# Optimization experiments

Hardware: AMD Instinct MI355X
Metric: run time of the kernel (lower is better)

The kernel has to match this reference:

```python
import jax, jax.numpy as jnp
import numpy as np

DIM = 192
HEADS = 8
B = 8
HH = 128
WW = 128
EPS_BN = 1e-5
EPS_NORM = 1e-12


def _bn(x, g, b, m, v):
    # inference-mode BatchNorm2d over channel axis 1, x: (B,C,H,W)
    inv = g / jnp.sqrt(v + EPS_BN)
    return x * inv[None, :, None, None] + (b - m * inv)[None, :, None, None]


def _gelu(x):
    return jax.nn.gelu(x, approximate=False)


def setup_inputs() -> dict:
    key = jax.random.key(0)
    ks = jax.random.split(key, 16)
    d, h8, h16 = DIM, DIM // 8, DIM // 16
    N = HH * WW
    s = 0.02
    inp = {
        "x": jax.random.normal(ks[0], (B, N, d), jnp.float32),
        "H": HH,
        "W": WW,
        "w_qkv": jax.random.normal(ks[1], (d, 3 * d), jnp.float32) * s,
        "temperature": jnp.ones((HEADS, 1, 1), jnp.float32),
        "dw_w": jax.random.normal(ks[2], (d, 1, 3, 3), jnp.float32) * s,
        "dw_b": jnp.zeros((d,), jnp.float32),
        "bn1_g": jnp.ones((d,), jnp.float32), "bn1_b": jnp.zeros((d,), jnp.float32),
        "bn1_m": jnp.zeros((d,), jnp.float32), "bn1_v": jnp.ones((d,), jnp.float32),
        "ci_w1": jax.random.normal(ks[3], (h8, d), jnp.float32) * s,
        "ci_b1": jnp.zeros((h8,), jnp.float32),
        "bn2_g": jnp.ones((h8,), jnp.float32), "bn2_b": jnp.zeros((h8,), jnp.float32),
        "bn2_m": jnp.zeros((h8,), jnp.float32), "bn2_v": jnp.ones((h8,), jnp.float32),
        "ci_w2": jax.random.normal(ks[4], (d, h8), jnp.float32) * s,
        "ci_b2": jnp.zeros((d,), jnp.float32),
        "si_w1": jax.random.normal(ks[5], (h16, d), jnp.float32) * s,
        "si_b1": jnp.zeros((h16,), jnp.float32),
        "bn3_g": jnp.ones((h16,), jnp.float32), "bn3_b": jnp.zeros((h16,), jnp.float32),
        "bn3_m": jnp.zeros((h16,), jnp.float32), "bn3_v": jnp.ones((h16,), jnp.float32),
        "si_w2": jax.random.normal(ks[6], (1, h16), jnp.float32) * s,
        "si_b2": jnp.zeros((1,), jnp.float32),
        "proj_w": jax.random.normal(ks[7], (d, d), jnp.float32) * s,
        "proj_b": jnp.zeros((d,), jnp.float32),
    }
    return inp


def reference(x, H, W, w_qkv, temperature, dw_w, dw_b,
              bn1_g, bn1_b, bn1_m, bn1_v,
              ci_w1, ci_b1, bn2_g, bn2_b, bn2_m, bn2_v, ci_w2, ci_b2,
              si_w1, si_b1, bn3_g, bn3_b, bn3_m, bn3_v, si_w2, si_b2,
              proj_w, proj_b):
    Bn, N, C = x.shape
    hd = C // HEADS
    # qkv projection (no bias), split into heads: (3,B,h,N,hd)
    qkv = (x @ w_qkv).reshape(Bn, N, 3, HEADS, hd).transpose(2, 0, 3, 1, 4)
    q = qkv[0].transpose(0, 1, 3, 2)  # (B,h,hd,N)
    k = qkv[1].transpose(0, 1, 3, 2)
    v = qkv[2].transpose(0, 1, 3, 2)
    v_img = v.reshape(Bn, C, N).reshape(Bn, C, H, W)
    # L2-normalize along token axis (F.normalize eps=1e-12)
    q = q / jnp.clip(jnp.linalg.norm(q, axis=-1, keepdims=True), EPS_NORM)
    k = k / jnp.clip(jnp.linalg.norm(k, axis=-1, keepdims=True), EPS_NORM)
    attn = jnp.einsum('bhcn,bhdn->bhcd', q, k) * temperature  # (B,h,hd,hd)
    attn = jax.nn.softmax(attn, axis=-1)
    att_x = jnp.einsum('bhcd,bhdn->bhcn', attn, v)  # (B,h,hd,N)
    att_x = att_x.transpose(0, 3, 1, 2).reshape(Bn, N, C)
    # depthwise conv branch: 3x3 dw conv + BN + GELU
    conv_x = jax.lax.conv_general_dilated(
        v_img, dw_w, window_strides=(1, 1), padding='SAME',
        dimension_numbers=('NCHW', 'OIHW', 'NCHW'), feature_group_count=C)
    conv_x = _gelu(_bn(conv_x + dw_b[None, :, None, None], bn1_g, bn1_b, bn1_m, bn1_v))
    # channel interaction: SE gate computed from attention branch
    att_img = att_x.transpose(0, 2, 1).reshape(Bn, C, H, W)
    pooled = jnp.mean(att_img, axis=(2, 3), keepdims=True)  # (B,C,1,1)
    cm = jnp.einsum('bcij,oc->boij', pooled, ci_w1) + ci_b1[None, :, None, None]
    cm = _gelu(_bn(cm, bn2_g, bn2_b, bn2_m, bn2_v))
    channel_map = jnp.einsum('bcij,oc->boij', cm, ci_w2) + ci_b2[None, :, None, None]
    # spatial interaction: gate computed from conv branch
    sm = jnp.einsum('bchw,oc->bohw', conv_x, si_w1) + si_b1[None, :, None, None]
    sm = _gelu(_bn(sm, bn3_g, bn3_b, bn3_m, bn3_v))
    spatial_map = jnp.einsum('bchw,oc->bohw', sm, si_w2) + si_b2[None, :, None, None]
    spatial_map = spatial_map.transpose(0, 2, 3, 1).reshape(Bn, N, 1)
    # cross gating
    att_x = att_x * jax.nn.sigmoid(spatial_map)
    conv_x = conv_x * jax.nn.sigmoid(channel_map)
    conv_x = conv_x.transpose(0, 2, 3, 1).reshape(Bn, N, C)
    out = (att_x + conv_x) @ proj_w + proj_b
    return out
```

## Files before the change

### kernel.cpp

```cpp
#include <hip/hip_runtime.h>
#include <math.h>

#define Bb 8
#define Cc 192
#define NHEADS 8
#define HDim 24
#define Him 128
#define Wim 128
#define Ntok 16384
#define EPSBN 1e-5f

typedef __bf16 bf16x8 __attribute__((ext_vector_type(8)));
typedef float  f32x4  __attribute__((ext_vector_type(4)));

static __device__ __forceinline__ float gelu_f(float v) {
    return 0.5f * v * (1.0f + erff(v * 0.70710678118654752f));
}
static __device__ __forceinline__ float sigmoid_f(float v) {
    return 1.0f / (1.0f + expf(-v));
}
static __device__ __forceinline__ void split8(const float* xv, bf16x8& h8, bf16x8& l8) {
#pragma unroll
    for (int j = 0; j < 8; ++j) {
        float v = xv[j];
        __bf16 h = (__bf16)v;
        h8[j] = h;
        l8[j] = (__bf16)(v - (float)h);
    }
}

__global__ __launch_bounds__(256) void k_wprep(const float* __restrict__ w,
                                               __bf16* __restrict__ wt)
{
    int idx = blockIdx.x * 256 + threadIdx.x;
    if (idx >= 36864) return;
    int k = idx / 192, c = idx % 192;
    float v = w[k * 576 + 384 + c];
    __bf16 h = (__bf16)v;
    __bf16 l = (__bf16)(v - (float)h);
    wt[c * 192 + k] = h;
    wt[36864 + c * 192 + k] = l;
}

__global__ __launch_bounds__(256, 2) void k_xtx(const float* __restrict__ x,
                                                float* __restrict__ xpart)
{
    const int t = threadIdx.x;
    const int lane = t & 63, wave = t >> 6;
    const int chunk = blockIdx.x;
    const int b = blockIdx.y;
    const int n0 = chunk * 256;
    const int m16 = lane & 15, q = lane >> 4;
    const int rq = (wave & 1) * 6;
    const int cq = (wave >> 1) * 6;

    f32x4 acc[6][6];
#pragma unroll
    for (int i = 0; i < 6; ++i)
#pragma unroll
        for (int j = 0; j < 6; ++j)
#pragma unroll
            for (int r = 0; r < 4; ++r) acc[i][j][r] = 0.f;

    const float* xb = x + ((size_t)b * Ntok + n0) * 192;

    for (int kt = 0; kt < 8; ++kt) {
        const float* base = xb + (size_t)(kt * 32 + q * 8) * 192 + m16;
#pragma unroll
        for (int rb = 0; rb < 2; ++rb) {
            bf16x8 fah[3], fal[3];
#pragma unroll
            for (int g = 0; g < 3; ++g) {
                const float* src = base + (rq + rb * 3 + g) * 16;
                float xv[8];
#pragma unroll
                for (int j = 0; j < 8; ++j) xv[j] = src[(size_t)j * 192];
                split8(xv, fah[g], fal[g]);
            }
#pragma unroll
            for (int cb = 0; cb < 2; ++cb) {
                bf16x8 fbh[3], fbl[3];
#pragma unroll
                for (int g = 0; g < 3; ++g) {
                    const float* src = base + (cq + cb * 3 + g) * 16;
                    float xv[8];
#pragma unroll
                    for (int j = 0; j < 8; ++j) xv[j] = src[(size_t)j * 192];
                    split8(xv, fbh[g], fbl[g]);
                }
#pragma unroll
                for (int ti = 0; ti < 3; ++ti)
#pragma unroll
                    for (int tj = 0; tj < 3; ++tj) {
                        f32x4& a = acc[rb * 3 + ti][cb * 3 + tj];
                        a = __builtin_amdgcn_mfma_f32_16x16x32_bf16(fah[ti], fbh[tj], a, 0, 0, 0);
                        a = __builtin_amdgcn_mfma_f32_16x16x32_bf16(fah[ti], fbl[tj], a, 0, 0, 0);
                        a = __builtin_amdgcn_mfma_f32_16x16x32_bf16(fal[ti], fbh[tj], a, 0, 0, 0);
                    }
            }
        }
    }
    float* op = xpart + ((size_t)b * 64 + chunk) * 36864;
#pragma unroll
    for (int ti = 0; ti < 6; ++ti)
#pragma unroll
        for (int tj = 0; tj < 6; ++tj) {
            const int row0 = (rq + ti) * 16 + q * 4;
            const int col = (cq + tj) * 16 + m16;
#pragma unroll
            for (int j = 0; j < 4; ++j)
                op[(size_t)(row0 + j) * 192 + col] = acc[ti][tj][j];
        }
}

__global__ __launch_bounds__(256) void k_xred(const float* __restrict__ xpart,
                                              float* __restrict__ XtX)
{
    const int b = blockIdx.y;
    const int e = blockIdx.x * 256 + threadIdx.x;
    const float* p = xpart + (size_t)b * 64 * 36864 + e;
    float s = 0.f;
#pragma unroll
    for (int c = 0; c < 64; ++c) s += p[(size_t)c * 36864];
    XtX[(size_t)b * 36864 + e] = s;
}

__global__ __launch_bounds__(256) void k_gram2(const float* __restrict__ XtX,
                                               const float* __restrict__ w_qkv,
                                               float* __restrict__ gram,
                                               float* __restrict__ ssq_q,
                                               float* __restrict__ ssq_k)
{
    __shared__ float wq[192][24];
    __shared__ float wk[192][24];
    __shared__ float U[192][24];
    __shared__ float V[192][24];
    const int b = blockIdx.x, h = blockIdx.y, t = threadIdx.x;
    for (int e = t; e < 4608; e += 256) {
        int k = e / 24, c = e % 24;
        wq[k][c] = w_qkv[k * 576 + h * 24 + c];
        wk[k][c] = w_qkv[k * 576 + 192 + h * 24 + c];
    }
    __syncthreads();
    if (t < 192) {
        const float* xr = XtX + (size_t)b * 36864 + (size_t)t * 192;
        float u[24], v[24];
#pragma unroll
        for (int c = 0; c < 24; ++c) { u[c] = 0.f; v[c] = 0.f; }
        for (int k4 = 0; k4 < 48; ++k4) {
            float4 x4 = *(const float4*)(xr + k4 * 4);
#pragma unroll
            for (int kk = 0; kk < 4; ++kk) {
                float xv = (&x4.x)[kk];
                int k = k4 * 4 + kk;
#pragma unroll
                for (int c = 0; c < 24; ++c) {
                    u[c] = fmaf(xv, wq[k][c], u[c]);
                    v[c] = fmaf(xv, wk[k][c], v[c]);
                }
            }
        }
#pragma unroll
        for (int c = 0; c < 24; ++c) { U[t][c] = u[c]; V[t][c] = v[c]; }
    }
    __syncthreads();
    for (int o = t; o < 576; o += 256) {
        int c = o / 24, d = o % 24;
        float g = 0.f;
        for (int r = 0; r < 192; ++r) g = fmaf(wq[r][c], V[r][d], g);
        gram[(size_t)(b * NHEADS + h) * 576 + o] = g;
    }
    if (t < 24) {
        float s = 0.f;
        for (int r = 0; r < 192; ++r) s = fmaf(wq[r][t], U[r][t], s);
        ssq_q[b * Cc + h * HDim + t] = s;
    } else if (t < 48) {
        int c = t - 24;
        float s = 0.f;
        for (int r = 0; r < 192; ++r) s = fmaf(wk[r][c], V[r][c], s);
        ssq_k[b * Cc + h * HDim + c] = s;
    }
}

__global__ __launch_bounds__(256, 2) void k_qkv_mfma(const float* __restrict__ x,
                                                     const __bf16* __restrict__ wt,
                                                     float* __restrict__ vout,
                                                     float* __restrict__ vsum)
{
    __shared__ __align__(16) __bf16 Ah[128 * 40];
    __shared__ __align__(16) __bf16 Al[128 * 40];
    __shared__ __align__(16) __bf16 Bh[192 * 40];
    __shared__ __align__(16) __bf16 Bl[192 * 40];

    const int t = threadIdx.x;
    const int lane = t & 63, wave = t >> 6;
    const int n0 = blockIdx.x * 128;
    const int b = blockIdx.y;
    const int row_base = (wave & 1) * 64;
    const int col_base = (wave >> 1) * 96;
    const int m16 = lane & 15, q = lane >> 4;

    f32x4 acc[4][6];
#pragma unroll
    for (int rt = 0; rt < 4; ++rt)
#pragma unroll
        for (int ct = 0; ct < 6; ++ct)
#pragma unroll
            for (int j = 0; j < 4; ++j) acc[rt][ct][j] = 0.f;

    const int ar = t >> 1, ahalf = t & 1;
    const float* xrow = x + ((size_t)b * Ntok + n0 + ar) * Cc + ahalf * 16;

    for (int kc = 0; kc < 6; ++kc) {
        {
            const float4* xp4 = (const float4*)(xrow + kc * 32);
            float xv[16];
            float4 u;
            u = xp4[0]; xv[0] = u.x; xv[1] = u.y; xv[2]  = u.z; xv[3]  = u.w;
            u = xp4[1]; xv[4] = u.x; xv[5] = u.y; xv[6]  = u.z; xv[7]  = u.w;
            u = xp4[2]; xv[8] = u.x; xv[9] = u.y; xv[10] = u.z; xv[11] = u.w;
            u = xp4[3]; xv[12] = u.x; xv[13] = u.y; xv[14] = u.z; xv[15] = u.w;
            bf16x8 vh0, vh1, vl0, vl1;
            split8(xv, vh0, vl0);
            split8(xv + 8, vh1, vl1);
            const int o = ar * 40 + ahalf * 16;
            *(bf16x8*)&Ah[o] = vh0; *(bf16x8*)&Ah[o + 8] = vh1;
            *(bf16x8*)&Al[o] = vl0; *(bf16x8*)&Al[o + 8] = vl1;
        }
#pragma unroll
        for (int i = 0; i < 3; ++i) {
            int f = i * 256 + t;
            int n = f >> 2, k8 = (f & 3) << 3;
            const __bf16* src = wt + (size_t)n * 192 + kc * 32 + k8;
            bf16x8 vh = *(const bf16x8*)src;
            bf16x8 vl = *(const bf16x8*)(src + 36864);
            *(bf16x8*)&Bh[n * 40 + k8] = vh;
            *(bf16x8*)&Bl[n * 40 + k8] = vl;
        }
        __syncthreads();

        bf16x8 fah[4], fal[4], fbh[6], fbl[6];
#pragma unroll
        for (int rt = 0; rt < 4; ++rt) {
            int o = (row_base + rt * 16 + m16) * 40 + q * 8;
            fah[rt] = *(const bf16x8*)&Ah[o];
            fal[rt] = *(const bf16x8*)&Al[o];
        }
#pragma unroll
        for (int ct = 0; ct < 6; ++ct) {
            int o = (col_base + ct * 16 + m16) * 40 + q * 8;
            fbh[ct] = *(const bf16x8*)&Bh[o];
            fbl[ct] = *(const bf16x8*)&Bl[o];
        }
#pragma unroll
        for (int rt = 0; rt < 4; ++rt)
#pragma unroll
            for (int ct = 0; ct < 6; ++ct) {
                acc[rt][ct] = __builtin_amdgcn_mfma_f32_16x16x32_bf16(
                    fah[rt], fbh[ct], acc[rt][ct], 0, 0, 0);
                acc[rt][ct] = __builtin_amdgcn_mfma_f32_16x16x32_bf16(
                    fah[rt], fbl[ct], acc[rt][ct], 0, 0, 0);
                acc[rt][ct] = __builtin_amdgcn_mfma_f32_16x16x32_bf16(
                    fal[rt], fbh[ct], acc[rt][ct], 0, 0, 0);
            }
        __syncthreads();
    }

    const size_t obase = (size_t)b * Cc * (size_t)Ntok;
#pragma unroll
    for (int rt = 0; rt < 4; ++rt)
#pragma unroll
        for (int ct = 0; ct < 6; ++ct) {
            int token = n0 + row_base + rt * 16 + q * 4;
            int col = col_base + ct * 16 + m16;
            float4 o = make_float4(acc[rt][ct][0], acc[rt][ct][1],
                                   acc[rt][ct][2], acc[rt][ct][3]);
            *(float4*)(vout + obase + (size_t)col * Ntok + token) = o;
        }

#pragma unroll
    for (int ct = 0; ct < 6; ++ct) {
        float s = 0.f;
#pragma unroll
        for (int rt = 0; rt < 4; ++rt)
            s += acc[rt][ct][0] + acc[rt][ct][1] + acc[rt][ct][2] + acc[rt][ct][3];
        s += __shfl_xor(s, 16, 64);
        s += __shfl_xor(s, 32, 64);
        if (q == 0)
            atomicAdd(vsum + b * Cc + col_base + ct * 16 + m16, s);
    }
}

__global__ __launch_bounds__(256) void k_attn(const float* __restrict__ gram,
                                              const float* __restrict__ ssq_q,
                                              const float* __restrict__ ssq_k,
                                              const float* __restrict__ temperature,
                                              const float* __restrict__ vmean,
                                              const float* __restrict__ ci_w1,
                                              const float* __restrict__ ci_b1,
                                              const float* __restrict__ bn2_g,
                                              const float* __restrict__ bn2_b,
                                              const float* __restrict__ bn2_m,
                                              const float* __restrict__ bn2_v,
                                              const float* __restrict__ ci_w2,
                                              const float* __restrict__ ci_b2,
                                              float* __restrict__ attn,
                                              float* __restrict__ sig_ch)
{
    __shared__ float pooled[192];
    __shared__ float cmv[24];
    const int b = blockIdx.x, t = threadIdx.x;
    if (t < 192) {
        int h = t / 24, c = t % 24;
        const float* gp = gram + (size_t)(b * NHEADS + h) * 576 + c * 24;
        float qn = fmaxf(sqrtf(ssq_q[b * Cc + h * HDim + c]), 1e-12f);
        float temp = temperature[h];
        float logit[24];
        float m = -1e30f;
#pragma unroll
        for (int d = 0; d < 24; ++d) {
            float kn = fmaxf(sqrtf(ssq_k[b * Cc + h * HDim + d]), 1e-12f);
            float l = gp[d] / (qn * kn) * temp;
            logit[d] = l; m = fmaxf(m, l);
        }
        float s = 0.f;
#pragma unroll
        for (int d = 0; d < 24; ++d) { float e = expf(logit[d] - m); logit[d] = e; s += e; }
        float inv = 1.f / s;
        float pool = 0.f;
        float* ap = attn + (size_t)(b * NHEADS + h) * 576 + c * 24;
#pragma unroll
        for (int d = 0; d < 24; ++d) {
            float a = logit[d] * inv;
            ap[d] = a;
            pool = fmaf(a, vmean[b * Cc + h * HDim + d], pool);
        }
        pooled[h * 24 + c] = pool * (1.0f / (float)Ntok);
    }
    __syncthreads();
    if (t < 24) {
        float z = ci_b1[t];
        for (int c = 0; c < 192; ++c) z = fmaf(ci_w1[t * 192 + c], pooled[c], z);
        float sc = bn2_g[t] / sqrtf(bn2_v[t] + EPSBN);
        z = z * sc + (bn2_b[t] - bn2_m[t] * sc);
        cmv[t] = gelu_f(z);
    }
    __syncthreads();
    if (t < 192) {
        float z = ci_b2[t];
#pragma unroll
        for (int o = 0; o < 24; ++o) z = fmaf(ci_w2[t * 24 + o], cmv[o], z);
        sig_ch[b * Cc + t] = sigmoid_f(z);
    }
}

__global__ __launch_bounds__(192) void k_pprep(const float* __restrict__ attn,
                                               const float* __restrict__ sig_ch,
                                               const float* __restrict__ proj_w,
                                               __bf16* __restrict__ Pt)
{
    const int b = blockIdx.x, part = blockIdx.y, j = threadIdx.x;
    __bf16* base = Pt + (size_t)b * (2 * 73728);
    if (part < 8) {
        const int h = part;
        __shared__ float at[576];
        for (int e = j; e < 576; e += 192) at[e] = attn[(size_t)(b * 8 + h) * 576 + e];
        __syncthreads();
        float pr[24];
#pragma unroll
        for (int cl = 0; cl < 24; ++cl) pr[cl] = proj_w[(h * 24 + cl) * 192 + j];
        float s[24];
#pragma unroll
        for (int d = 0; d < 24; ++d) s[d] = 0.f;
#pragma unroll
        for (int cl = 0; cl < 24; ++cl) {
            float a = pr[cl];
#pragma unroll
            for (int d = 0; d < 24; ++d) s[d] = fmaf(a, at[cl * 24 + d], s[d]);
        }
#pragma unroll
        for (int d = 0; d < 24; ++d) {
            float v = s[d];
            __bf16 hi = (__bf16)v;
            base[j * 384 + h * 24 + d] = hi;
            base[73728 + j * 384 + h * 24 + d] = (__bf16)(v - (float)hi);
        }
    } else {
        __shared__ float sch_s[192];
        sch_s[j] = sig_ch[b * Cc + j];
        __syncthreads();
        for (int ch = 0; ch < 192; ++ch) {
            float v = sch_s[ch] * proj_w[ch * 192 + j];
            __bf16 hi = (__bf16)v;
            base[j * 384 + 192 + ch] = hi;
            base[73728 + j * 384 + 192 + ch] = (__bf16)(v - (float)hi);
        }
    }
}

__global__ __launch_bounds__(256) void k_conv(const float* __restrict__ vbuf,
                                              const float* __restrict__ dw_w,
                                              const float* __restrict__ dw_b,
                                              const float* __restrict__ bn1_g,
                                              const float* __restrict__ bn1_b,
                                              const float* __restrict__ bn1_m,
                                              const float* __restrict__ bn1_v,
                                              float* __restrict__ convx)
{
    __shared__ float vh[8][10][130];
    __shared__ float dww[8 * 9];
    __shared__ float scl[8], shf[8];
    const int t = threadIdx.x;
    const int y0 = blockIdx.x * 8;
    const int ch0 = blockIdx.y * 8;
    const int b = blockIdx.z;

    if (t < 72) {
        dww[t] = dw_w[ch0 * 9 + t];
    } else if (t < 80) {
        int c = t - 72, ch = ch0 + c;
        float sc = bn1_g[ch] / sqrtf(bn1_v[ch] + EPSBN);
        scl[c] = sc;
        shf[c] = (dw_b[ch] - bn1_m[ch]) * sc + bn1_b[ch];
    } else if (t < 160) {
        int e = t - 80;
        int ch = e / 10, r = e % 10;
        vh[ch][r][0] = 0.f;
        vh[ch][r][129] = 0.f;
    }
    for (int e = t; e < 8 * 10 * 128; e += 256) {
        int ch = e / 1280, rem = e - ch * 1280;
        int r = rem >> 7, xc = rem & 127;
        int gy = y0 - 1 + r;
        float v = 0.f;
        if (gy >= 0 && gy < Him)
            v = vbuf[((size_t)b * Cc + ch0 + ch) * Ntok + gy * Wim + xc];
        vh[ch][r][xc + 1] = v;
    }
    __syncthreads();

    const int xc = t & 127, half = t >> 7;
#pragma unroll
    for (int ch = 0; ch < 8; ++ch) {
        const float w0 = dww[ch * 9 + 0], w1 = dww[ch * 9 + 1], w2 = dww[ch * 9 + 2];
        const float w3 = dww[ch * 9 + 3], w4 = dww[ch * 9 + 4], w5 = dww[ch * 9 + 5];
        const float w6 = dww[ch * 9 + 6], w7 = dww[ch * 9 + 7], w8 = dww[ch * 9 + 8];
        const float sc = scl[ch], sh = shf[ch];
        float* op = convx + ((size_t)b * Cc + ch0 + ch) * Ntok + (size_t)y0 * Wim + xc;
#pragma unroll
        for (int rr = 0; rr < 4; ++rr) {
            int r = half * 4 + rr;
            const float* r0 = &vh[ch][r][xc];
            const float* r1 = &vh[ch][r + 1][xc];
            const float* r2 = &vh[ch][r + 2][xc];
            float conv = r0[0] * w0 + r0[1] * w1 + r0[2] * w2
                       + r1[0] * w3 + r1[1] * w4 + r1[2] * w5
                       + r2[0] * w6 + r2[1] * w7 + r2[2] * w8;
            op[(size_t)r * Wim] = gelu_f(conv * sc + sh);
        }
    }
}

__global__ __launch_bounds__(256, 2) void k_final_mfma(const float* __restrict__ vbuf,
                                                       const float* __restrict__ convx,
                                                       const __bf16* __restrict__ Pt,
                                                       const float* __restrict__ si_w1,
                                                       const float* __restrict__ si_b1,
                                                       const float* __restrict__ bn3_g,
                                                       const float* __restrict__ bn3_b,
                                                       const float* __restrict__ bn3_m,
                                                       const float* __restrict__ bn3_v,
                                                       const float* __restrict__ si_w2,
                                                       const float* __restrict__ si_b2,
                                                       const float* __restrict__ proj_b,
                                                       float* __restrict__ out)
{
    __shared__ __align__(16) __bf16 Ah[128 * 40];
    __shared__ __align__(16) __bf16 Al[128 * 40];
    __shared__ __align__(16) __bf16 Bh[192 * 40];
    __shared__ __align__(16) __bf16 Bl[192 * 40];
    __shared__ float smbuf[128][17];
    __shared__ float ssp_s[128];

    const int t = threadIdx.x;
    const int lane = t & 63, wave = t >> 6;
    const int n0 = blockIdx.x * 128;
    const int b = blockIdx.y;
    const int row_base = (wave & 1) * 64;
    const int col_base = (wave >> 1) * 96;
    const int m16 = lane & 15, q = lane >> 4;

    const int an = t & 127;
    const int akh = (t >> 7) & 1;
    const __bf16* ptb = Pt + (size_t)b * (2 * 73728);

    f32x4 acc[4][6];
#pragma unroll
    for (int rt = 0; rt < 4; ++rt)
#pragma unroll
        for (int ct = 0; ct < 6; ++ct)
#pragma unroll
            for (int j = 0; j < 4; ++j) acc[rt][ct][j] = 0.f;
    f32x4 accS[4];
#pragma unroll
    for (int rt = 0; rt < 4; ++rt)
#pragma unroll
        for (int j = 0; j < 4; ++j) accS[rt][j] = 0.f;

    for (int phase = 0; phase < 2; ++phase) {
        if (phase == 1) {
#pragma unroll
            for (int rt = 0; rt < 4; ++rt) {
                int row = row_base + rt * 16 + q * 4;
#pragma unroll
                for (int j = 0; j < 4; ++j)
                    smbuf[row + j][m16] = accS[rt][j];
            }
            __syncthreads();
            if (t < 128) {
                float sp = si_b2[0];
#pragma unroll
                for (int o = 0; o < 12; ++o) {
                    float z = smbuf[t][o] + si_b1[o];
                    float sc = bn3_g[o] / sqrtf(bn3_v[o] + EPSBN);
                    z = z * sc + (bn3_b[o] - bn3_m[o] * sc);
                    sp = fmaf(si_w2[o], gelu_f(z), sp);
                }
                ssp_s[t] = sigmoid_f(sp);
            }
            __syncthreads();
        }
        for (int ki = 0; ki < 6; ++ki) {
            const int kc = (phase == 0) ? (ki + 6) : ki;
            {
                const int ch0 = ki * 32 + akh * 16;
                const float* src;
                float scale;
                if (phase == 0) {
                    src = convx + ((size_t)b * Cc + ch0) * Ntok + n0 + an;
                    scale = 1.f;
                } else {
                    src = vbuf + ((size_t)b * Cc + ch0) * Ntok + n0 + an;
                    scale = ssp_s[an];
                }
                float xv[16];
#pragma unroll
                for (int jj = 0; jj < 16; ++jj)
                    xv[jj] = src[(size_t)jj * Ntok] * scale;
                bf16x8 vh0, vl0, vh1, vl1;
                split8(xv, vh0, vl0);
                split8(xv + 8, vh1, vl1);
                const int o = an * 40 + akh * 16;
                *(bf16x8*)&Ah[o] = vh0; *(bf16x8*)&Ah[o + 8] = vh1;
                *(bf16x8*)&Al[o] = vl0; *(bf16x8*)&Al[o + 8] = vl1;
            }
#pragma unroll
            for (int i = 0; i < 3; ++i) {
                int f = i * 256 + t;
                int col = f >> 2, k8 = (f & 3) << 3;
                const __bf16* sp = ptb + (size_t)col * 384 + kc * 32 + k8;
                bf16x8 vh = *(const bf16x8*)sp;
                bf16x8 vl = *(const bf16x8*)(sp + 73728);
                *(bf16x8*)&Bh[col * 40 + k8] = vh;
                *(bf16x8*)&Bl[col * 40 + k8] = vl;
            }
            __syncthreads();

            bf16x8 fah[4], fal[4], fbh[6], fbl[6];
#pragma unroll
            for (int rt = 0; rt < 4; ++rt) {
                int o = (row_base + rt * 16 + m16) * 40 + q * 8;
                fah[rt] = *(const bf16x8*)&Ah[o];
                fal[rt] = *(const bf16x8*)&Al[o];
            }
#pragma unroll
            for (int ct = 0; ct < 6; ++ct) {
                int o = (col_base + ct * 16 + m16) * 40 + q * 8;
                fbh[ct] = *(const bf16x8*)&Bh[o];
            }
#pragma unroll
            for (int rt = 0; rt < 4; ++rt)
#pragma unroll
                for (int ct = 0; ct < 6; ++ct) {
                    acc[rt][ct] = __builtin_amdgcn_mfma_f32_16x16x32_bf16(
                        fah[rt], fbh[ct], acc[rt][ct], 0, 0, 0);
                    acc[rt][ct] = __builtin_amdgcn_mfma_f32_16x16x32_bf16(
                        fal[rt], fbh[ct], acc[rt][ct], 0, 0, 0);
                }
#pragma unroll
            for (int ct = 0; ct < 6; ++ct) {
                int o = (col_base + ct * 16 + m16) * 40 + q * 8;
                fbl[ct] = *(const bf16x8*)&Bl[o];
            }
#pragma unroll
            for (int rt = 0; rt < 4; ++rt)
#pragma unroll
                for (int ct = 0; ct < 6; ++ct)
                    acc[rt][ct] = __builtin_amdgcn_mfma_f32_16x16x32_bf16(
                        fah[rt], fbl[ct], acc[rt][ct], 0, 0, 0);

            if (phase == 0) {
                bf16x8 w1h, w1l;
                if (m16 < 12) {
                    const float* wp = si_w1 + m16 * 192 + ki * 32 + q * 8;
                    float wv[8];
                    float4 u0 = *(const float4*)wp, u1 = *(const float4*)(wp + 4);
                    wv[0] = u0.x; wv[1] = u0.y; wv[2] = u0.z; wv[3] = u0.w;
                    wv[4] = u1.x; wv[5] = u1.y; wv[6] = u1.z; wv[7] = u1.w;
                    split8(wv, w1h, w1l);
                } else {
#pragma unroll
                    for (int j = 0; j < 8; ++j) { w1h[j] = (__bf16)0.f; w1l[j] = (__bf16)0.f; }
                }
#pragma unroll
                for (int rt = 0; rt < 4; ++rt) {
                    accS[rt] = __builtin_amdgcn_mfma_f32_16x16x32_bf16(
                        fah[rt], w1h, accS[rt], 0, 0, 0);
                    accS[rt] = __builtin_amdgcn_mfma_f32_16x16x32_bf16(
                        fal[rt], w1h, accS[rt], 0, 0, 0);
                    accS[rt] = __builtin_amdgcn_mfma_f32_16x16x32_bf16(
                        fah[rt], w1l, accS[rt], 0, 0, 0);
                }
            }
            __syncthreads();
        }
    }

    float* ob = out + ((size_t)b * Ntok + n0) * Cc;
#pragma unroll
    for (int ct = 0; ct < 6; ++ct) {
        const int col = col_base + ct * 16 + m16;
        const float pbv = proj_b[col];
#pragma unroll
        for (int rt = 0; rt < 4; ++rt) {
            const int row = row_base + rt * 16 + q * 4;
#pragma unroll
            for (int j = 0; j < 4; ++j)
                ob[(size_t)(row + j) * Cc + col] = acc[rt][ct][j] + pbv;
        }
    }
}

extern "C" void kernel_launch(void* const* d_in, const int* in_sizes, int n_in,
                              void* d_out, int out_size, void* d_ws, size_t ws_size,
                              hipStream_t stream)
{
    const float* x      = (const float*)d_in[0];
    const float* w_qkv  = (const float*)d_in[3];
    const float* temperature = (const float*)d_in[4];
    const float* dw_w   = (const float*)d_in[5];
    const float* dw_b   = (const float*)d_in[6];
    const float* bn1_g  = (const float*)d_in[7];
    const float* bn1_b  = (const float*)d_in[8];
    const float* bn1_m  = (const float*)d_in[9];
    const float* bn1_v  = (const float*)d_in[10];
    const float* ci_w1  = (const float*)d_in[11];
    const float* ci_b1  = (const float*)d_in[12];
    const float* bn2_g  = (const float*)d_in[13];
    const float* bn2_b  = (const float*)d_in[14];
    const float* bn2_m  = (const float*)d_in[15];
    const float* bn2_v  = (const float*)d_in[16];
    const float* ci_w2  = (const float*)d_in[17];
    const float* ci_b2  = (const float*)d_in[18];
    const float* si_w1  = (const float*)d_in[19];
    const float* si_b1  = (const float*)d_in[20];
    const float* bn3_g  = (const float*)d_in[21];
    const float* bn3_b  = (const float*)d_in[22];
    const float* bn3_m  = (const float*)d_in[23];
    const float* bn3_v  = (const float*)d_in[24];
    const float* si_w2  = (const float*)d_in[25];
    const float* si_b2  = (const float*)d_in[26];
    const float* proj_w = (const float*)d_in[27];
    const float* proj_b = (const float*)d_in[28];

    float* ws = (float*)d_ws;
    const size_t BCN = (size_t)Bb * Cc * Ntok;
    float* vbuf  = ws;
    float* convx = ws + BCN;
    __bf16* Pt   = (__bf16*)(ws + 2 * BCN);
    float* xpart = ws + 2 * BCN + 589824;
    float* XtX   = xpart + 18874368;
    float* gram  = XtX + 294912;
    float* ssq_q = gram + 36864;
    float* ssq_k = ssq_q + 1536;
    float* vmean = ssq_k + 1536;
    float* attn  = vmean + 1536;
    float* sig_ch = attn + 36864;
    float* out = (float*)d_out;

    __bf16* wt = (__bf16*)(out + BCN - 36864);

    hipMemsetAsync(vmean, 0, 1536 * sizeof(float), stream);

    k_wprep<<<dim3(144), 256, 0, stream>>>(w_qkv, wt);
    k_xtx<<<dim3(64, Bb), 256, 0, stream>>>(x, xpart);
    k_xred<<<dim3(144, Bb), 256, 0, stream>>>(xpart, XtX);
    k_gram2<<<dim3(Bb, NHEADS), 256, 0, stream>>>(XtX, w_qkv, gram, ssq_q, ssq_k);
    k_qkv_mfma<<<dim3(Ntok / 128, Bb), 256, 0, stream>>>(x, wt, vbuf, vmean);
    k_attn<<<dim3(Bb), 256, 0, stream>>>(gram, ssq_q, ssq_k, temperature, vmean,
                                         ci_w1, ci_b1, bn2_g, bn2_b, bn2_m, bn2_v,
                                         ci_w2, ci_b2, attn, sig_ch);
    k_pprep<<<dim3(Bb, 9), 192, 0, stream>>>(attn, sig_ch, proj_w, Pt);
    k_conv<<<dim3(Him / 8, Cc / 8, Bb), 256, 0, stream>>>(
        vbuf, dw_w, dw_b, bn1_g, bn1_b, bn1_m, bn1_v, convx);
    k_final_mfma<<<dim3(Ntok / 128, Bb), 256, 0, stream>>>(
        vbuf, convx, Pt, si_w1, si_b1, bn3_g, bn3_b, bn3_m, bn3_v,
        si_w2, si_b2, proj_b, out);
}
```

Baseline: 610.3 us.

## Stage XtX tiles through LDS with coalesced loads; vectorize depthwise conv

The X^T X kernel now loads x with coalesced float4 reads, splits each value into bf16 hi/lo once, and stores the result transposed in shared memory. The MFMA fragments are then read from shared memory instead of as strided scalar global loads that were each split several times. Each block covers 512 tokens instead of 256, which halves the partial-sum buffer and the reduction work but launches fewer blocks. The depthwise conv drops its shared-memory halo tile: each thread reads its three rows directly with float4 loads and writes four outputs as one float4.

```diff
diff --git a/kernel.cpp b/kernel.cpp
--- a/kernel.cpp
+++ b/kernel.cpp
@@ -11,6 +11,7 @@
 #define EPSBN 1e-5f
 
 typedef __bf16 bf16x8 __attribute__((ext_vector_type(8)));
+typedef __bf16 bf16x2 __attribute__((ext_vector_type(2)));
 typedef float  f32x4  __attribute__((ext_vector_type(4)));
 
 static __device__ __forceinline__ float gelu_f(float v) {
@@ -45,11 +46,13 @@
 __global__ __launch_bounds__(256, 2) void k_xtx(const float* __restrict__ x,
                                                 float* __restrict__ xpart)
 {
+    __shared__ __align__(16) __bf16 Th[192 * 40];
+    __shared__ __align__(16) __bf16 Tl[192 * 40];
     const int t = threadIdx.x;
     const int lane = t & 63, wave = t >> 6;
     const int chunk = blockIdx.x;
     const int b = blockIdx.y;
-    const int n0 = chunk * 256;
+    const int n0 = chunk * 512;
     const int m16 = lane & 15, q = lane >> 4;
     const int rq = (wave & 1) * 6;
     const int cq = (wave >> 1) * 6;
@@ -62,31 +65,61 @@
 #pragma unroll
             for (int r = 0; r < 4; ++r) acc[i][j][r] = 0.f;
 
+    int u0 = t, u1 = t + 256, u2 = t + 512;
+    const int ch4_0 = (u0 % 48) * 4, tk_0 = (u0 / 48) * 2;
+    const int ch4_1 = (u1 % 48) * 4, tk_1 = (u1 / 48) * 2;
+    const int ch4_2 = (u2 % 48) * 4, tk_2 = (u2 / 48) * 2;
     const float* xb = x + ((size_t)b * Ntok + n0) * 192;
-
-    for (int kt = 0; kt < 8; ++kt) {
-        const float* base = xb + (size_t)(kt * 32 + q * 8) * 192 + m16;
+    const float* p0 = xb + (size_t)tk_0 * 192 + ch4_0;
+    const float* p1 = xb + (size_t)tk_1 * 192 + ch4_1;
+    const float* p2 = xb + (size_t)tk_2 * 192 + ch4_2;
+    const int o0 = ch4_0 * 40 + tk_0;
+    const int o1 = ch4_1 * 40 + tk_1;
+    const int o2 = ch4_2 * 40 + tk_2;
+
+    for (int ks = 0; ks < 16; ++ks) {
+        __syncthreads();
+        {
+            const float* pp[3] = { p0, p1, p2 };
+            const int oo[3] = { o0, o1, o2 };
+#pragma unroll
+            for (int j = 0; j < 3; ++j) {
+                const float* p = pp[j] + (size_t)ks * 32 * 192;
+                float4 a = *(const float4*)p;
+                float4 c = *(const float4*)(p + 192);
+#pragma unroll
+                for (int cix = 0; cix < 4; ++cix) {
+                    float v0 = (&a.x)[cix], v1 = (&c.x)[cix];
+                    __bf16 h0 = (__bf16)v0, h1 = (__bf16)v1;
+                    __bf16 l0 = (__bf16)(v0 - (float)h0);
+                    __bf16 l1 = (__bf16)(v1 - (float)h1);
+                    int o = oo[j] + cix * 40;
+                    bf16x2 hp; hp[0] = h0; hp[1] = h1;
+                    bf16x2 lp; lp[0] = l0; lp[1] = l1;
+                    *(bf16x2*)&Th[o] = hp;
+                    *(bf16x2*)&Tl[o] = lp;
+                }
+            }
+        }
+        __syncthreads();
+
 #pragma unroll
         for (int rb = 0; rb < 2; ++rb) {
             bf16x8 fah[3], fal[3];
 #pragma unroll
             for (int g = 0; g < 3; ++g) {
-                const float* src = base + (rq + rb * 3 + g) * 16;
-                float xv[8];
-#pragma unroll
-                for (int j = 0; j < 8; ++j) xv[j] = src[(size_t)j * 192];
-                split8(xv, fah[g], fal[g]);
+                int o = ((rq + rb * 3 + g) * 16 + m16) * 40 + q * 8;
+                fah[g] = *(const bf16x8*)&Th[o];
+                fal[g] = *(const bf16x8*)&Tl[o];
             }
 #pragma unroll
             for (int cb = 0; cb < 2; ++cb) {
                 bf16x8 fbh[3], fbl[3];
 #pragma unroll
                 for (int g = 0; g < 3; ++g) {
-                    const float* src = base + (cq + cb * 3 + g) * 16;
-                    float xv[8];
-#pragma unroll
-                    for (int j = 0; j < 8; ++j) xv[j] = src[(size_t)j * 192];
-                    split8(xv, fbh[g], fbl[g]);
+                    int o = ((cq + cb * 3 + g) * 16 + m16) * 40 + q * 8;
+                    fbh[g] = *(const bf16x8*)&Th[o];
+                    fbl[g] = *(const bf16x8*)&Tl[o];
                 }
 #pragma unroll
                 for (int ti = 0; ti < 3; ++ti)
@@ -100,7 +133,7 @@
             }
         }
     }
-    float* op = xpart + ((size_t)b * 64 + chunk) * 36864;
+    float* op = xpart + ((size_t)b * 32 + chunk) * 36864;
 #pragma unroll
     for (int ti = 0; ti < 6; ++ti)
 #pragma unroll
@@ -118,10 +151,10 @@
 {
     const int b = blockIdx.y;
     const int e = blockIdx.x * 256 + threadIdx.x;
-    const float* p = xpart + (size_t)b * 64 * 36864 + e;
+    const float* p = xpart + (size_t)b * 32 * 36864 + e;
     float s = 0.f;
 #pragma unroll
-    for (int c = 0; c < 64; ++c) s += p[(size_t)c * 36864];
+    for (int c = 0; c < 32; ++c) s += p[(size_t)c * 36864];
     XtX[(size_t)b * 36864 + e] = s;
 }
 
@@ -407,8 +440,7 @@
                                               const float* __restrict__ bn1_v,
                                               float* __restrict__ convx)
 {
-    __shared__ float vh[8][10][130];
-    __shared__ float dww[8 * 9];
+    __shared__ float dww[72];
     __shared__ float scl[8], shf[8];
     const int t = threadIdx.x;
     const int y0 = blockIdx.x * 8;
@@ -422,42 +454,45 @@
         float sc = bn1_g[ch] / sqrtf(bn1_v[ch] + EPSBN);
         scl[c] = sc;
         shf[c] = (dw_b[ch] - bn1_m[ch]) * sc + bn1_b[ch];
-    } else if (t < 160) {
-        int e = t - 80;
-        int ch = e / 10, r = e % 10;
-        vh[ch][r][0] = 0.f;
-        vh[ch][r][129] = 0.f;
-    }
-    for (int e = t; e < 8 * 10 * 128; e += 256) {
-        int ch = e / 1280, rem = e - ch * 1280;
-        int r = rem >> 7, xc = rem & 127;
-        int gy = y0 - 1 + r;
-        float v = 0.f;
-        if (gy >= 0 && gy < Him)
-            v = vbuf[((size_t)b * Cc + ch0 + ch) * Ntok + gy * Wim + xc];
-        vh[ch][r][xc + 1] = v;
     }
     __syncthreads();
 
-    const int xc = t & 127, half = t >> 7;
+    const int xq = (t & 31) * 4;
+    const int r = t >> 5;
+    const int gy = y0 + r;
+
 #pragma unroll
     for (int ch = 0; ch < 8; ++ch) {
+        const float* base = vbuf + ((size_t)b * Cc + ch0 + ch) * Ntok;
+        float v[3][6];
+#pragma unroll
+        for (int dy = 0; dy < 3; ++dy) {
+            int iy = gy - 1 + dy;
+            if (iy >= 0 && iy < Him) {
+                const float* rp = base + (size_t)iy * Wim;
+                float4 m = *(const float4*)(rp + xq);
+                v[dy][1] = m.x; v[dy][2] = m.y; v[dy][3] = m.z; v[dy][4] = m.w;
+                v[dy][0] = (xq > 0) ? rp[xq - 1] : 0.f;
+                v[dy][5] = (xq < 124) ? rp[xq + 4] : 0.f;
+            } else {
+#pragma unroll
+                for (int i2 = 0; i2 < 6; ++i2) v[dy][i2] = 0.f;
+            }
+        }
         const float w0 = dww[ch * 9 + 0], w1 = dww[ch * 9 + 1], w2 = dww[ch * 9 + 2];
         const float w3 = dww[ch * 9 + 3], w4 = dww[ch * 9 + 4], w5 = dww[ch * 9 + 5];
         const float w6 = dww[ch * 9 + 6], w7 = dww[ch * 9 + 7], w8 = dww[ch * 9 + 8];
         const float sc = scl[ch], sh = shf[ch];
-        float* op = convx + ((size_t)b * Cc + ch0 + ch) * Ntok + (size_t)y0 * Wim + xc;
-#pragma unroll
-        for (int rr = 0; rr < 4; ++rr) {
-            int r = half * 4 + rr;
-            const float* r0 = &vh[ch][r][xc];
-            const float* r1 = &vh[ch][r + 1][xc];
-            const float* r2 = &vh[ch][r + 2][xc];
-            float conv = r0[0] * w0 + r0[1] * w1 + r0[2] * w2
-                       + r1[0] * w3 + r1[1] * w4 + r1[2] * w5
-                       + r2[0] * w6 + r2[1] * w7 + r2[2] * w8;
-            op[(size_t)r * Wim] = gelu_f(conv * sc + sh);
-        }
+        float4 o;
+#pragma unroll
+        for (int p = 0; p < 4; ++p) {
+            float s = v[0][p] * w0 + v[0][p + 1] * w1 + v[0][p + 2] * w2
+                    + v[1][p] * w3 + v[1][p + 1] * w4 + v[1][p + 2] * w5
+                    + v[2][p] * w6 + v[2][p + 1] * w7 + v[2][p + 2] * w8;
+            (&o.x)[p] = gelu_f(s * sc + sh);
+        }
+        *(float4*)(convx + ((size_t)b * Cc + ch0 + ch) * Ntok
+                   + (size_t)gy * Wim + xq) = o;
     }
 }
 
@@ -679,7 +714,7 @@
     float* convx = ws + BCN;
     __bf16* Pt   = (__bf16*)(ws + 2 * BCN);
     float* xpart = ws + 2 * BCN + 589824;
-    float* XtX   = xpart + 18874368;
+    float* XtX   = xpart + 9437184;
     float* gram  = XtX + 294912;
     float* ssq_q = gram + 36864;
     float* ssq_k = ssq_q + 1536;
@@ -693,7 +728,7 @@
     hipMemsetAsync(vmean, 0, 1536 * sizeof(float), stream);
 
     k_wprep<<<dim3(144), 256, 0, stream>>>(w_qkv, wt);
-    k_xtx<<<dim3(64, Bb), 256, 0, stream>>>(x, xpart);
+    k_xtx<<<dim3(32, Bb), 256, 0, stream>>>(x, xpart);
     k_xred<<<dim3(144, Bb), 256, 0, stream>>>(xpart, XtX);
     k_gram2<<<dim3(Bb, NHEADS), 256, 0, stream>>>(XtX, w_qkv, gram, ssq_q, ssq_k);
     k_qkv_mfma<<<dim3(Ntok / 128, Bb), 256, 0, stream>>>(x, wt, vbuf, vmean);
```

Measured after the change: 559.6 us. 1.09x faster.
